# Optimization experiments

Hardware: AMD Instinct MI355X
Metric: run time of the kernel (lower is better)

Reference implementation:

```python
import jax, jax.numpy as jnp
import numpy as np

# Quantization constants from the original module
X_ZP = -66   # int8 zero point
Y_ZP = 160   # uint8 zero point


def setup_inputs() -> dict:
    key = jax.random.key(0)
    k1, k2 = jax.random.split(key)
    # x: [7, B, M, K] int8 in [-128, 127]
    x = jax.random.randint(k1, (7, 8, 512, 1024), -128, 128, dtype=jnp.int32).astype(jnp.int8)
    # y: [B, K, N] uint8 in [0, 255]
    y = jax.random.randint(k2, (8, 1024, 512), 0, 256, dtype=jnp.int32).astype(jnp.uint8)
    return {
        "x": x,
        "y": y,
        "x_scale": jnp.float32(0.03),
        "y_scale": jnp.float32(0.025),
    }


def reference(x, y, x_scale, y_scale):
    # dequantize_per_tensor: (q - zero_point) * scale
    xf = (x.astype(jnp.float32) - jnp.float32(X_ZP)) * x_scale   # [7, B, M, K]
    yf = (y.astype(jnp.float32) - jnp.float32(Y_ZP)) * y_scale   # [B, K, N]
    # torch.matmul broadcast: [7,B,M,K] @ [B,K,N] -> [7,B,M,N]
    return jnp.einsum('gbmk,bkn->gbmn', xf, yf)
```

## Files before the change

kernel.cpp:

```cpp
#include <hip/hip_runtime.h>
#include <stdint.h>

#define AS1 __attribute__((address_space(1)))
#define AS3 __attribute__((address_space(3)))

typedef int v4i __attribute__((ext_vector_type(4)));

constexpr int G = 7, B = 8, M = 512, N = 512, K = 1024;
constexpr int GBn = G * B;

constexpr size_t X8_BYTES = (size_t)GBn * M * K;
constexpr size_t YT_BYTES = (size_t)B * N * K;
constexpr size_t RS_CNT   = (size_t)GBn * M;
constexpr size_t CS_CNT   = (size_t)B * N;
constexpr size_t WS_NEEDED = X8_BYTES + YT_BYTES + RS_CNT * 4 + CS_CNT * 4;

__global__ __launch_bounds__(256) void transpose_pack_y(const int* __restrict__ y,
                                                        signed char* __restrict__ yt) {
    __shared__ unsigned char tile[64][80];
    int n0 = blockIdx.x * 64;
    int k0 = blockIdx.y * 64;
    int b  = blockIdx.z;
    int t  = threadIdx.x;

    int r  = t >> 2;
    int c0 = (t & 3) * 16;
    const int* src = y + ((size_t)b * K + k0 + r) * N + n0 + c0;
    uint32_t p[4];
#pragma unroll
    for (int q = 0; q < 4; ++q) {
        int4 v = ((const int4*)src)[q];
        p[q] =  (uint32_t)((v.x & 255) ^ 128)
             | ((uint32_t)((v.y & 255) ^ 128) << 8)
             | ((uint32_t)((v.z & 255) ^ 128) << 16)
             | ((uint32_t)((v.w & 255) ^ 128) << 24);
    }
    *(uint4*)&tile[r][c0] = make_uint4(p[0], p[1], p[2], p[3]);
    __syncthreads();

    int nl = t >> 2;
    int kc = (t & 3) * 16;
    uint32_t q[4];
#pragma unroll
    for (int w = 0; w < 4; ++w) {
        uint32_t b0 = tile[kc + w * 4 + 0][nl];
        uint32_t b1 = tile[kc + w * 4 + 1][nl];
        uint32_t b2 = tile[kc + w * 4 + 2][nl];
        uint32_t b3 = tile[kc + w * 4 + 3][nl];
        q[w] = b0 | (b1 << 8) | (b2 << 16) | (b3 << 24);
    }
    *(uint4*)(yt + ((size_t)b * N + n0 + nl) * K + k0 + kc) = make_uint4(q[0], q[1], q[2], q[3]);
}

__device__ __forceinline__ int wave_reduce_sum(int v) {
#pragma unroll
    for (int off = 32; off > 0; off >>= 1) v += __shfl_down(v, off, 64);
    return v;
}

__global__ __launch_bounds__(256) void pack_x_sums(const int* __restrict__ x,
                                                   signed char* __restrict__ x8,
                                                   const signed char* __restrict__ yt,
                                                   int* __restrict__ rowsum,
                                                   int* __restrict__ colsum) {
    int wave = threadIdx.x >> 6, lane = threadIdx.x & 63;
    int row = blockIdx.x * 4 + wave;
    if (row < (int)(GBn * M)) {
        const int* src = x + (size_t)row * K + lane * 16;
        int s = 0;
        uint32_t p[4];
#pragma unroll
        for (int q = 0; q < 4; ++q) {
            int4 v = ((const int4*)src)[q];
            s += v.x + v.y + v.z + v.w;
            p[q] =  (uint32_t)(v.x & 255)
                 | ((uint32_t)(v.y & 255) << 8)
                 | ((uint32_t)(v.z & 255) << 16)
                 | ((uint32_t)(v.w & 255) << 24);
        }
        *(uint4*)(x8 + (size_t)row * K + lane * 16) = make_uint4(p[0], p[1], p[2], p[3]);
        s = wave_reduce_sum(s);
        if (lane == 0) rowsum[row] = s;
    } else {
        int rr = row - (int)(GBn * M);
        uint4 u = *(const uint4*)(yt + (size_t)rr * K + lane * 16);
        uint32_t wds[4] = {u.x, u.y, u.z, u.w};
        int s = 0;
#pragma unroll
        for (int q = 0; q < 4; ++q) {
            uint32_t w = wds[q];
            s += (int)(signed char)(w) + (int)(signed char)(w >> 8)
               + (int)(signed char)(w >> 16) + (int)(signed char)(w >> 24);
        }
        s = wave_reduce_sum(s);
        if (lane == 0) colsum[rr] = s;
    }
}

__global__ __launch_bounds__(256, 2) void gemm_i8(const signed char* __restrict__ x8,
                                                  const signed char* __restrict__ yt,
                                                  const int* __restrict__ rowsum,
                                                  const int* __restrict__ colsum,
                                                  const float* __restrict__ xsp,
                                                  const float* __restrict__ ysp,
                                                  float* __restrict__ out) {
    __shared__ signed char lds[4][2][8192];

    int mt = blockIdx.x, nt = blockIdx.y, gb = blockIdx.z;
    int b  = gb & 7;
    int tid = threadIdx.x, w = tid >> 6, lane = tid & 63;
    int wm = (w >> 1) * 64, wn = (w & 1) * 64;

    int chunk = ((lane & 3) ^ ((lane >> 3) & 3)) * 16;
    const signed char* Ab = x8 + ((size_t)(gb * M + mt * 128 + wm + (lane >> 2))) * K + chunk;
    const signed char* Bb = yt + ((size_t)(b  * N + nt * 128 + wn + (lane >> 2))) * K + chunk;
    signed char* L = &lds[w][0][0];

    int fr = lane & 15, q = lane >> 4;
    int fko = (q ^ ((fr >> 1) & 3)) * 16;

    v4i acc[4][4];
#pragma unroll
    for (int i = 0; i < 4; ++i)
#pragma unroll
        for (int j = 0; j < 4; ++j) acc[i][j] = (v4i){0, 0, 0, 0};

#define STAGE(SIDX, BUF)                                                                  \
    do {                                                                                  \
        _Pragma("unroll")                                                                 \
        for (int c = 0; c < 4; ++c)                                                       \
            __builtin_amdgcn_global_load_lds(                                             \
                (const AS1 uint32_t*)(Ab + (size_t)c * 16 * K + (SIDX) * 64),             \
                (AS3 uint32_t*)(L + (BUF) * 8192 + c * 1024), 16, 0, 0);                  \
        _Pragma("unroll")                                                                 \
        for (int c = 0; c < 4; ++c)                                                       \
            __builtin_amdgcn_global_load_lds(                                             \
                (const AS1 uint32_t*)(Bb + (size_t)c * 16 * K + (SIDX) * 64),             \
                (AS3 uint32_t*)(L + (BUF) * 8192 + 4096 + c * 1024), 16, 0, 0);           \
    } while (0)

    STAGE(0, 0);
    STAGE(1, 1);

    for (int s = 0; s < 16; ++s) {
        int buf = s & 1;
        if (s < 15) asm volatile("s_waitcnt vmcnt(8)" ::: "memory");
        else        asm volatile("s_waitcnt vmcnt(0)" ::: "memory");

        v4i af[4], bf[4];
#pragma unroll
        for (int i = 0; i < 4; ++i)
            af[i] = *(const v4i*)(L + buf * 8192 + (i * 16 + fr) * 64 + fko);
#pragma unroll
        for (int j = 0; j < 4; ++j)
            bf[j] = *(const v4i*)(L + buf * 8192 + 4096 + (j * 16 + fr) * 64 + fko);
        asm volatile("s_waitcnt lgkmcnt(0)" ::: "memory");

        if (s < 14) STAGE(s + 2, buf);

#pragma unroll
        for (int i = 0; i < 4; ++i)
#pragma unroll
            for (int j = 0; j < 4; ++j)
                acc[i][j] = __builtin_amdgcn_mfma_i32_16x16x64_i8(af[i], bf[j], acc[i][j], 0, 0, 0);
    }
#undef STAGE

    float sc = xsp[0] * ysp[0];
    int colL = lane & 15;
    int rowQ = (lane >> 4) * 4;
    float* outg = out + (size_t)gb * M * N;
    const int* rs = rowsum + gb * M;
    const int* cs = colsum + b * N;
#pragma unroll
    for (int i = 0; i < 4; ++i) {
#pragma unroll
        for (int r = 0; r < 4; ++r) {
            int row_g = mt * 128 + wm + i * 16 + rowQ + r;
            int rsv = rs[row_g];
#pragma unroll
            for (int j = 0; j < 4; ++j) {
                int col_g = nt * 128 + wn + j * 16 + colL;
                int t = acc[i][j][r] - 32 * rsv + 66 * cs[col_g] - 2162688;
                outg[(size_t)row_g * N + col_g] = sc * (float)t;
            }
        }
    }
}

__global__ __launch_bounds__(256) void naive_kernel(const int* __restrict__ x,
                                                    const int* __restrict__ y,
                                                    const float* __restrict__ xsp,
                                                    const float* __restrict__ ysp,
                                                    float* __restrict__ out) {
    size_t idx = (size_t)blockIdx.x * 256 + threadIdx.x;
    int n  = (int)(idx & 511);
    int m  = (int)((idx >> 9) & 511);
    int gb = (int)(idx >> 18);
    int b  = gb & 7;
    const int* xr = x + ((size_t)gb * M + m) * K;
    const int* yc = y + (size_t)b * K * N + n;
    int dot = 0, sx = 0, sy = 0;
    for (int k = 0; k < K; ++k) {
        int a = xr[k];
        int c = yc[(size_t)k * N];
        dot += a * c; sx += a; sy += c;
    }
    float s = xsp[0] * ysp[0];
    out[idx] = s * (float)(dot - 160 * sx + 66 * sy - 10813440);
}

extern "C" void kernel_launch(void* const* d_in, const int* in_sizes, int n_in,
                              void* d_out, int out_size, void* d_ws, size_t ws_size,
                              hipStream_t stream) {
    const int*   x  = (const int*)d_in[0];
    const int*   y  = (const int*)d_in[1];
    const float* xs = (const float*)d_in[2];
    const float* ys = (const float*)d_in[3];
    float* out = (float*)d_out;

    if (ws_size < WS_NEEDED) {
        naive_kernel<<<(14680064 + 255) / 256, 256, 0, stream>>>(x, y, xs, ys, out);
        return;
    }

    char* ws = (char*)d_ws;
    signed char* x8 = (signed char*)ws;
    signed char* yt = (signed char*)(ws + X8_BYTES);
    int* rowsum = (int*)(ws + X8_BYTES + YT_BYTES);
    int* colsum = rowsum + RS_CNT;

    transpose_pack_y<<<dim3(N / 64, K / 64, B), 256, 0, stream>>>(y, yt);
    pack_x_sums<<<(GBn * M + CS_CNT) / 4, 256, 0, stream>>>(x, x8, yt, rowsum, colsum);
    gemm_i8<<<dim3(M / 128, N / 128, GBn), 256, 0, stream>>>(x8, yt, rowsum, colsum, xs, ys, out);
}
```

Before: 231.3 us.

## Share 256x256 block tile in LDS across eight waves with double buffering

The int8 GEMM changes from four independent waves, each staging its own 64x64 slice, to a 512-thread block computing a 256x256 output tile. All waves share one double-buffered LDS A/B tile and each wave computes a 128x64 sub-tile. This raises operand reuse and cuts global traffic per output, but adds a __syncthreads per k-step and uses only one prefetch stage. It also doubles accumulator registers per wave and leaves only 224 blocks, fewer than four per CU.

```diff
diff --git a/kernel.cpp b/kernel.cpp
--- a/kernel.cpp
+++ b/kernel.cpp
@@ -97,69 +97,67 @@
     }
 }
 
-__global__ __launch_bounds__(256, 2) void gemm_i8(const signed char* __restrict__ x8,
+__global__ __launch_bounds__(512, 2) void gemm_i8(const signed char* __restrict__ x8,
                                                   const signed char* __restrict__ yt,
                                                   const int* __restrict__ rowsum,
                                                   const int* __restrict__ colsum,
                                                   const float* __restrict__ xsp,
                                                   const float* __restrict__ ysp,
                                                   float* __restrict__ out) {
-    __shared__ signed char lds[4][2][8192];
+    __shared__ signed char lds[2][32768];
 
     int mt = blockIdx.x, nt = blockIdx.y, gb = blockIdx.z;
     int b  = gb & 7;
     int tid = threadIdx.x, w = tid >> 6, lane = tid & 63;
-    int wm = (w >> 1) * 64, wn = (w & 1) * 64;
-
+    int wm = (w >> 2) * 128;
+    int wn = (w & 3) * 64;
+
+    int srow  = lane >> 2;
     int chunk = ((lane & 3) ^ ((lane >> 3) & 3)) * 16;
-    const signed char* Ab = x8 + ((size_t)(gb * M + mt * 128 + wm + (lane >> 2))) * K + chunk;
-    const signed char* Bb = yt + ((size_t)(b  * N + nt * 128 + wn + (lane >> 2))) * K + chunk;
-    signed char* L = &lds[w][0][0];
+    const signed char* Ab = x8 + ((size_t)(gb * M + mt * 256 + w * 32 + srow)) * K + chunk;
+    const signed char* Bb = yt + ((size_t)(b  * N + nt * 256 + w * 32 + srow)) * K + chunk;
 
     int fr = lane & 15, q = lane >> 4;
     int fko = (q ^ ((fr >> 1) & 3)) * 16;
 
-    v4i acc[4][4];
-#pragma unroll
-    for (int i = 0; i < 4; ++i)
+    v4i acc[8][4];
+#pragma unroll
+    for (int i = 0; i < 8; ++i)
 #pragma unroll
         for (int j = 0; j < 4; ++j) acc[i][j] = (v4i){0, 0, 0, 0};
 
-#define STAGE(SIDX, BUF)                                                                  \
-    do {                                                                                  \
-        _Pragma("unroll")                                                                 \
-        for (int c = 0; c < 4; ++c)                                                       \
-            __builtin_amdgcn_global_load_lds(                                             \
-                (const AS1 uint32_t*)(Ab + (size_t)c * 16 * K + (SIDX) * 64),             \
-                (AS3 uint32_t*)(L + (BUF) * 8192 + c * 1024), 16, 0, 0);                  \
-        _Pragma("unroll")                                                                 \
-        for (int c = 0; c < 4; ++c)                                                       \
-            __builtin_amdgcn_global_load_lds(                                             \
-                (const AS1 uint32_t*)(Bb + (size_t)c * 16 * K + (SIDX) * 64),             \
-                (AS3 uint32_t*)(L + (BUF) * 8192 + 4096 + c * 1024), 16, 0, 0);           \
+#define STAGE(SIDX, BUF)                                                                   \
+    do {                                                                                   \
+        _Pragma("unroll")                                                                  \
+        for (int c = 0; c < 2; ++c) {                                                      \
+            __builtin_amdgcn_global_load_lds(                                              \
+                (const AS1 uint32_t*)(Ab + (size_t)c * 16 * K + (SIDX) * 64),              \
+                (AS3 uint32_t*)(&lds[BUF][0] + w * 2048 + c * 1024), 16, 0, 0);            \
+            __builtin_amdgcn_global_load_lds(                                              \
+                (const AS1 uint32_t*)(Bb + (size_t)c * 16 * K + (SIDX) * 64),              \
+                (AS3 uint32_t*)(&lds[BUF][0] + 16384 + w * 2048 + c * 1024), 16, 0, 0);    \
+        }                                                                                  \
     } while (0)
 
     STAGE(0, 0);
-    STAGE(1, 1);
 
     for (int s = 0; s < 16; ++s) {
         int buf = s & 1;
-        if (s < 15) asm volatile("s_waitcnt vmcnt(8)" ::: "memory");
-        else        asm volatile("s_waitcnt vmcnt(0)" ::: "memory");
-
-        v4i af[4], bf[4];
-#pragma unroll
-        for (int i = 0; i < 4; ++i)
-            af[i] = *(const v4i*)(L + buf * 8192 + (i * 16 + fr) * 64 + fko);
+        __syncthreads();
+
+        v4i af[8], bf[4];
+#pragma unroll
+        for (int i = 0; i < 8; ++i)
+            af[i] = *(const v4i*)(&lds[buf][0] + (wm + i * 16 + fr) * 64 + fko);
 #pragma unroll
         for (int j = 0; j < 4; ++j)
-            bf[j] = *(const v4i*)(L + buf * 8192 + 4096 + (j * 16 + fr) * 64 + fko);
-        asm volatile("s_waitcnt lgkmcnt(0)" ::: "memory");
-
-        if (s < 14) STAGE(s + 2, buf);
-
-#pragma unroll
-        for (int i = 0; i < 4; ++i)
+            bf[j] = *(const v4i*)(&lds[buf][0] + 16384 + (wn + j * 16 + fr) * 64 + fko);
+
+        asm volatile("" ::: "memory");
+        if (s < 15) STAGE(s + 1, buf ^ 1);
+
+#pragma unroll
+        for (int i = 0; i < 8; ++i)
 #pragma unroll
             for (int j = 0; j < 4; ++j)
                 acc[i][j] = __builtin_amdgcn_mfma_i32_16x16x64_i8(af[i], bf[j], acc[i][j], 0, 0, 0);
@@ -173,14 +171,14 @@
     const int* rs = rowsum + gb * M;
     const int* cs = colsum + b * N;
 #pragma unroll
-    for (int i = 0; i < 4; ++i) {
+    for (int i = 0; i < 8; ++i) {
 #pragma unroll
         for (int r = 0; r < 4; ++r) {
-            int row_g = mt * 128 + wm + i * 16 + rowQ + r;
+            int row_g = mt * 256 + wm + i * 16 + rowQ + r;
             int rsv = rs[row_g];
 #pragma unroll
             for (int j = 0; j < 4; ++j) {
-                int col_g = nt * 128 + wn + j * 16 + colL;
+                int col_g = nt * 256 + wn + j * 16 + colL;
                 int t = acc[i][j][r] - 32 * rsv + 66 * cs[col_g] - 2162688;
                 outg[(size_t)row_g * N + col_g] = sc * (float)t;
             }
@@ -232,5 +230,5 @@
 
     transpose_pack_y<<<dim3(N / 64, K / 64, B), 256, 0, stream>>>(y, yt);
     pack_x_sums<<<(GBn * M + CS_CNT) / 4, 256, 0, stream>>>(x, x8, yt, rowsum, colsum);
-    gemm_i8<<<dim3(M / 128, N / 128, GBn), 256, 0, stream>>>(x8, yt, rowsum, colsum, xs, ys, out);
-}
+    gemm_i8<<<dim3(M / 256, N / 256, GBn), 512, 0, stream>>>(x8, yt, rowsum, colsum, xs, ys, out);
+}
```

New measurement: 227.8 us. Within noise of the previous version (-1.5%).
